# Performance work log

Measured on AMD Instinct MI355X. Metric: run time of the kernel, lower is better.

Reference implementation:

```python
import jax, jax.numpy as jnp
import numpy as np

# Static configuration (mirrors TemporalAugmentation with deterministic choices)
B, T_IN, N, C = 32, 512, 543, 3
SPEED = 1.2                      # fixed draw from speed_range (0.8, 1.2)
NEW_T = int(T_IN / SPEED)        # 426
JITTER_FREQ = max(1, NEW_T // 8) # 53
FRAME_DROP_P = 0.1
JITTER_STD = 0.02
NOISE_STD = 0.01
SPATIAL_STD = 0.005


def linresample(x, out_T):
    """F.interpolate(mode='linear', align_corners=True) along last axis."""
    L = x.shape[-1]
    s = jnp.arange(out_T, dtype=x.dtype) * ((L - 1) / (out_T - 1))
    i0 = jnp.clip(jnp.floor(s).astype(jnp.int32), 0, L - 2)
    frac = s - i0.astype(x.dtype)
    return x[..., i0] * (1 - frac) + x[..., i0 + 1] * frac


def setup_inputs() -> dict:
    key = jax.random.key(0)
    k1, k2, k3, k4, k5 = jax.random.split(key, 5)
    x = jax.random.normal(k1, (B, T_IN, N, C), dtype=jnp.float32)
    mask = jnp.ones((B, T_IN), dtype=bool)
    keep_mask = jax.random.bernoulli(k2, 1.0 - FRAME_DROP_P, (B, NEW_T))
    keep_mask = keep_mask.at[:, 0].set(True).at[:, -1].set(True)
    base_jitter = jax.random.normal(k3, (B, JITTER_FREQ), dtype=jnp.float32)
    noise = jax.random.normal(k4, (B, NEW_T, N, C), dtype=jnp.float32)
    spatial_noise = jax.random.normal(k5, (B, 1, N, C), dtype=jnp.float32)
    return {"x": x, "mask": mask, "keep_mask": keep_mask,
            "base_jitter": base_jitter, "noise": noise,
            "spatial_noise": spatial_noise}


def reference(x, mask, keep_mask, base_jitter, noise, spatial_noise):
    Bb, T, Nn, Cc = x.shape
    # --- speed augment: linear resample time axis T -> NEW_T ---
    xt = jnp.moveaxis(x, 1, -1)                 # (B,N,C,T)
    x = jnp.moveaxis(linresample(xt, NEW_T), -1, 1)  # (B,NEW_T,N,C)
    # nearest resample of validity mask (PyTorch 'nearest': floor(t*in/out))
    nidx = jnp.floor(jnp.arange(NEW_T) * (T / NEW_T)).astype(jnp.int32)
    mask = mask[:, nidx]
    T2 = NEW_T
    # --- frame dropout: replace dropped frames with align_corners linear
    # resample of the kept-frame subsequence (length K) back to T2 ---
    K = keep_mask.sum(axis=1)                   # (B,) kept counts
    ar = jnp.arange(T2)
    # stable order putting kept indices first, in original order
    order = jnp.argsort(jnp.where(keep_mask, ar, T2 + ar), axis=1)  # (B,T2)
    s = ar[None, :].astype(x.dtype) * (K[:, None] - 1).astype(x.dtype) / (T2 - 1)
    r0 = jnp.clip(jnp.floor(s).astype(jnp.int32), 0, (K - 2)[:, None])
    frac = (s - r0.astype(x.dtype))[:, :, None, None]
    bidx = jnp.arange(Bb)[:, None]
    idx0 = jnp.take_along_axis(order, r0, axis=1)
    idx1 = jnp.take_along_axis(order, r0 + 1, axis=1)
    interp = x[bidx, idx0] * (1 - frac) + x[bidx, idx1] * frac
    x = jnp.where(keep_mask[:, :, None, None], x, interp)
    mask = mask & keep_mask
    # --- temporal jitter: scale per-frame velocity by smooth jitter curve ---
    jit = linresample(base_jitter * JITTER_STD, T2)   # (B,T2)
    vel = x[:, 1:] - x[:, :-1]
    x = jnp.concatenate([x[:, :1], x[:, 1:] + vel * jit[:, 1:, None, None]], axis=1)
    # --- coordinate noise + per-landmark spatial noise ---
    x = x + noise * NOISE_STD + spatial_noise * SPATIAL_STD
    return x, mask
```

## Files before the change

kernel.cpp:

```cpp
#include <hip/hip_runtime.h>
#include <stdint.h>

#define B_      32
#define T_IN_   512
#define N_      543
#define C_      3
#define NEW_T_  426
#define JF_     53
#define NC_     (N_*C_)
#define XOUT_   (B_*NEW_T_*NC_)
#define NGROUP_ (XOUT_/4)

#define MODE_INT   0
#define MODE_BYTE  1
#define MODE_FLOAT 2

typedef float f4u __attribute__((vector_size(16), aligned(4)));

__device__ __forceinline__ bool read_flag(const void* p, int mode, int idx) {
    if (mode == MODE_BYTE)  return ((const uint8_t*)p)[idx] != 0;
    if (mode == MODE_FLOAT) return ((const float*)p)[idx]   != 0.0f;
    return ((const int*)p)[idx] != 0;
}

__global__ __launch_bounds__(512) void prep_kernel(
    const void* __restrict__ maskp,
    const void* __restrict__ keepp,
    const float* __restrict__ bjit,
    float* __restrict__ out_mask,
    int4*  __restrict__ wsF,
    float4* __restrict__ wsW,
    float* __restrict__ wsJ)
{
    const int b = blockIdx.x;
    const int tid = threadIdx.x;

    __shared__ int flags[6];
    __shared__ int s_mode_mask, s_mode_keep;
    if (tid < 6) flags[tid] = 0;
    __syncthreads();
    if (tid < 64) {
        uint32_t vm = ((const uint32_t*)maskp)[tid];
        uint32_t vk = ((const uint32_t*)keepp)[tid];
        if (vm == 0x3F800000u)      atomicOr(&flags[2], 1);
        else if (vm > 1u)           atomicOr(&flags[1], 1);
        if (vk == 0x3F800000u)      atomicOr(&flags[5], 1);
        else if (vk > 1u)           atomicOr(&flags[4], 1);
    }
    __syncthreads();
    if (tid == 0) {
        s_mode_mask = flags[2] ? MODE_FLOAT : (flags[1] ? MODE_BYTE : MODE_INT);
        s_mode_keep = flags[5] ? MODE_FLOAT : (flags[4] ? MODE_BYTE : MODE_INT);
    }
    __syncthreads();
    const int mmode = s_mode_mask, kmode = s_mode_keep;

    __shared__ int sk[512];
    __shared__ int ps[512];
    __shared__ int kept[NEW_T_];

    int kv = 0;
    if (tid < NEW_T_) kv = read_flag(keepp, kmode, b*NEW_T_ + tid) ? 1 : 0;
    sk[tid] = (tid < NEW_T_) ? kv : 0;
    ps[tid] = sk[tid];
    __syncthreads();
    for (int off = 1; off < 512; off <<= 1) {
        int v = (tid >= off) ? ps[tid - off] : 0;
        __syncthreads();
        ps[tid] += v;
        __syncthreads();
    }
    const int K = ps[NEW_T_ - 1];
    if (tid < NEW_T_ && kv) kept[ps[tid] - 1] = tid;
    __syncthreads();

    if (tid < NEW_T_) {
        const int t = tid;
        const float RATX = (float)(511.0 / 425.0);
        float st = (float)t * RATX;
        int i0 = (int)floorf(st);
        if (i0 < 0) i0 = 0; if (i0 > T_IN_ - 2) i0 = T_IN_ - 2;
        float w = st - (float)i0;

        int4 F; float4 W;
        if (kv) {
            F = make_int4(i0, i0 + 1, i0, i0 + 1);
            W = make_float4(1.0f - w, w, 0.0f, 0.0f);
        } else {
            float s = ((float)t * (float)(K - 1)) / 425.0f;
            int r0 = (int)floorf(s);
            if (r0 < 0) r0 = 0; if (r0 > K - 2) r0 = K - 2;
            float f = s - (float)r0;
            int j0 = kept[r0], j1 = kept[r0 + 1];
            float s0 = (float)j0 * RATX;
            int a0 = (int)floorf(s0);
            if (a0 < 0) a0 = 0; if (a0 > T_IN_ - 2) a0 = T_IN_ - 2;
            float w0 = s0 - (float)a0;
            float s1 = (float)j1 * RATX;
            int a1 = (int)floorf(s1);
            if (a1 < 0) a1 = 0; if (a1 > T_IN_ - 2) a1 = T_IN_ - 2;
            float w1 = s1 - (float)a1;
            F = make_int4(a0, a0 + 1, a1, a1 + 1);
            W = make_float4((1.0f - f) * (1.0f - w0), (1.0f - f) * w0,
                            f * (1.0f - w1),          f * w1);
        }
        const int bt = b * NEW_T_ + t;
        wsF[bt] = F;
        wsW[bt] = W;

        const float RATJ = (float)(52.0 / 425.0);
        float sj = (float)t * RATJ;
        int ji = (int)floorf(sj);
        if (ji < 0) ji = 0; if (ji > JF_ - 2) ji = JF_ - 2;
        float jf = sj - (float)ji;
        float b0 = bjit[b*JF_ + ji]     * 0.02f;
        float b1 = bjit[b*JF_ + ji + 1] * 0.02f;
        float jv = b0 * (1.0f - jf) + b1 * jf;
        if (t == 0) jv = 0.0f;
        wsJ[bt] = jv;

        float mn = (float)t * (float)(512.0 / 426.0);
        int nidx = (int)floorf(mn);
        if (nidx > T_IN_ - 1) nidx = T_IN_ - 1;
        bool mo = read_flag(maskp, mmode, b*T_IN_ + nidx) && (kv != 0);
        out_mask[bt] = mo ? 1.0f : 0.0f;
    }
}

__global__ __launch_bounds__(256) void main_kernel(
    const float* __restrict__ x,
    const float* __restrict__ noise,
    const float* __restrict__ spat,
    const int4*  __restrict__ wsF,
    const float4* __restrict__ wsW,
    const float* __restrict__ wsJ,
    float* __restrict__ out)
{
    uint32_t g = blockIdx.x * 256u + threadIdx.x;
    if (g >= (uint32_t)NGROUP_) return;
    uint32_t flat = g * 4u;
    uint32_t bt = flat / (uint32_t)NC_;
    uint32_t e  = flat - bt * (uint32_t)NC_;

    if (e <= (uint32_t)(NC_ - 4)) {
        uint32_t b = bt / (uint32_t)NEW_T_;
        const float* xb = x + (size_t)b * (T_IN_ * NC_);
        int4  F  = wsF[bt];  float4 W  = wsW[bt];
        uint32_t pbt = bt ? bt - 1u : 0u;
        int4  FP = wsF[pbt]; float4 WP = wsW[pbt];
        float jv = wsJ[bt];

        f4u t0 = *(const f4u*)(xb + (uint32_t)F.x  * NC_ + e);
        f4u t1 = *(const f4u*)(xb + (uint32_t)F.y  * NC_ + e);
        f4u t2 = *(const f4u*)(xb + (uint32_t)F.z  * NC_ + e);
        f4u t3 = *(const f4u*)(xb + (uint32_t)F.w  * NC_ + e);
        f4u q0 = *(const f4u*)(xb + (uint32_t)FP.x * NC_ + e);
        f4u q1 = *(const f4u*)(xb + (uint32_t)FP.y * NC_ + e);
        f4u q2 = *(const f4u*)(xb + (uint32_t)FP.z * NC_ + e);
        f4u q3 = *(const f4u*)(xb + (uint32_t)FP.w * NC_ + e);
        f4u nz = *(const f4u*)(noise + flat);
        f4u sp = *(const f4u*)(spat + b * NC_ + e);

        f4u a  = W.x  * t0 + W.y  * t1 + W.z  * t2 + W.w  * t3;
        f4u ap = WP.x * q0 + WP.y * q1 + WP.z * q2 + WP.w * q3;
        f4u r  = a + (a - ap) * jv + nz * 0.01f + sp * 0.005f;
        *(f4u*)(out + flat) = r;
    } else {
        #pragma unroll
        for (int i = 0; i < 4; i++) {
            uint32_t fl  = flat + i;
            uint32_t bt2 = fl / (uint32_t)NC_;
            uint32_t e2  = fl - bt2 * (uint32_t)NC_;
            uint32_t b2  = bt2 / (uint32_t)NEW_T_;
            const float* xb = x + (size_t)b2 * (T_IN_ * NC_);
            int4  F  = wsF[bt2];  float4 W  = wsW[bt2];
            uint32_t pbt = bt2 ? bt2 - 1u : 0u;
            int4  FP = wsF[pbt];  float4 WP = wsW[pbt];
            float jv = wsJ[bt2];
            float a  = W.x  * xb[(uint32_t)F.x  * NC_ + e2] + W.y  * xb[(uint32_t)F.y  * NC_ + e2]
                     + W.z  * xb[(uint32_t)F.z  * NC_ + e2] + W.w  * xb[(uint32_t)F.w  * NC_ + e2];
            float ap = WP.x * xb[(uint32_t)FP.x * NC_ + e2] + WP.y * xb[(uint32_t)FP.y * NC_ + e2]
                     + WP.z * xb[(uint32_t)FP.z * NC_ + e2] + WP.w * xb[(uint32_t)FP.w * NC_ + e2];
            out[fl] = a + (a - ap) * jv + noise[fl] * 0.01f + spat[b2 * NC_ + e2] * 0.005f;
        }
    }
}

extern "C" void kernel_launch(void* const* d_in, const int* in_sizes, int n_in,
                              void* d_out, int out_size, void* d_ws, size_t ws_size,
                              hipStream_t stream) {
    const float* x    = (const float*)d_in[0];
    const void*  mask = d_in[1];
    const void*  keep = d_in[2];
    const float* bjit = (const float*)d_in[3];
    const float* noise = (const float*)d_in[4];
    const float* spat  = (const float*)d_in[5];
    float* out = (float*)d_out;

    char* ws = (char*)d_ws;
    int4*   wsF = (int4*)ws;
    float4* wsW = (float4*)(ws + 218112);
    float*  wsJ = (float*)(ws + 436224);

    prep_kernel<<<B_, 512, 0, stream>>>(mask, keep, bjit,
                                        out + XOUT_, wsF, wsW, wsJ);
    const int nblk = (NGROUP_ + 255) / 256;
    main_kernel<<<nblk, 256, 0, stream>>>(x, noise, spat, wsF, wsW, wsJ, out);
}
```

Before: 273.3 us.

## Process four per-frame groups per thread with batched loads and frame-aligned indexing

Reworks the main kernel so each thread handles four 4-element groups strided across the grid. All weight, index and data loads are issued first, then the math and stores run. Indexing is now per frame: 408 groups per frame, with the last group clamped so it overlaps and rewrites three elements, which removes the scalar tail path. Integer divisions become multiply-shift reciprocals, and a waves-per-eu hint is added. The aim is more memory-level parallelism per thread and less index arithmetic, at the cost of higher register pressure and some redundant overlapping writes.

```diff
diff --git a/kernel.cpp b/kernel.cpp
--- a/kernel.cpp
+++ b/kernel.cpp
@@ -9,7 +9,11 @@
 #define JF_     53
 #define NC_     (N_*C_)
 #define XOUT_   (B_*NEW_T_*NC_)
-#define NGROUP_ (XOUT_/4)
+#define NFR_    (B_*NEW_T_)
+#define GPF_    408
+#define TOTG_   (NFR_*GPF_)
+#define G_      4
+#define NBLK_   5432
 
 #define MODE_INT   0
 #define MODE_BYTE  1
@@ -127,7 +131,8 @@
     }
 }
 
-__global__ __launch_bounds__(256) void main_kernel(
+__global__ __launch_bounds__(256) __attribute__((amdgpu_waves_per_eu(2, 8)))
+void main_kernel(
     const float* __restrict__ x,
     const float* __restrict__ noise,
     const float* __restrict__ spat,
@@ -136,53 +141,56 @@
     const float* __restrict__ wsJ,
     float* __restrict__ out)
 {
-    uint32_t g = blockIdx.x * 256u + threadIdx.x;
-    if (g >= (uint32_t)NGROUP_) return;
-    uint32_t flat = g * 4u;
-    uint32_t bt = flat / (uint32_t)NC_;
-    uint32_t e  = flat - bt * (uint32_t)NC_;
-
-    if (e <= (uint32_t)(NC_ - 4)) {
-        uint32_t b = bt / (uint32_t)NEW_T_;
-        const float* xb = x + (size_t)b * (T_IN_ * NC_);
-        int4  F  = wsF[bt];  float4 W  = wsW[bt];
+    const uint32_t S = NBLK_ * 256u;
+    const uint32_t g0 = blockIdx.x * 256u + threadIdx.x;
+
+    int4   F[G_], FP[G_];
+    float4 W[G_], WP[G_];
+    float  JV[G_];
+    uint32_t E0[G_], BT[G_], BB[G_];
+    bool   VA[G_];
+
+    #pragma unroll
+    for (int k = 0; k < G_; k++) {
+        uint32_t gid = g0 + (uint32_t)k * S;
+        bool v = gid < (uint32_t)TOTG_;
+        VA[k] = v;
+        uint32_t gc = v ? gid : 0u;
+        uint32_t bt = (uint32_t)(((uint64_t)gc * 673720361ull) >> 38);
+        uint32_t j  = gc - bt * (uint32_t)GPF_;
+        uint32_t e0 = j * 4u; if (e0 > (uint32_t)(NC_ - 4)) e0 = (uint32_t)(NC_ - 4);
+        uint32_t b  = (uint32_t)(((uint64_t)bt * 161313326ull) >> 36);
         uint32_t pbt = bt ? bt - 1u : 0u;
-        int4  FP = wsF[pbt]; float4 WP = wsW[pbt];
-        float jv = wsJ[bt];
-
-        f4u t0 = *(const f4u*)(xb + (uint32_t)F.x  * NC_ + e);
-        f4u t1 = *(const f4u*)(xb + (uint32_t)F.y  * NC_ + e);
-        f4u t2 = *(const f4u*)(xb + (uint32_t)F.z  * NC_ + e);
-        f4u t3 = *(const f4u*)(xb + (uint32_t)F.w  * NC_ + e);
-        f4u q0 = *(const f4u*)(xb + (uint32_t)FP.x * NC_ + e);
-        f4u q1 = *(const f4u*)(xb + (uint32_t)FP.y * NC_ + e);
-        f4u q2 = *(const f4u*)(xb + (uint32_t)FP.z * NC_ + e);
-        f4u q3 = *(const f4u*)(xb + (uint32_t)FP.w * NC_ + e);
-        f4u nz = *(const f4u*)(noise + flat);
-        f4u sp = *(const f4u*)(spat + b * NC_ + e);
-
-        f4u a  = W.x  * t0 + W.y  * t1 + W.z  * t2 + W.w  * t3;
-        f4u ap = WP.x * q0 + WP.y * q1 + WP.z * q2 + WP.w * q3;
-        f4u r  = a + (a - ap) * jv + nz * 0.01f + sp * 0.005f;
-        *(f4u*)(out + flat) = r;
-    } else {
-        #pragma unroll
-        for (int i = 0; i < 4; i++) {
-            uint32_t fl  = flat + i;
-            uint32_t bt2 = fl / (uint32_t)NC_;
-            uint32_t e2  = fl - bt2 * (uint32_t)NC_;
-            uint32_t b2  = bt2 / (uint32_t)NEW_T_;
-            const float* xb = x + (size_t)b2 * (T_IN_ * NC_);
-            int4  F  = wsF[bt2];  float4 W  = wsW[bt2];
-            uint32_t pbt = bt2 ? bt2 - 1u : 0u;
-            int4  FP = wsF[pbt];  float4 WP = wsW[pbt];
-            float jv = wsJ[bt2];
-            float a  = W.x  * xb[(uint32_t)F.x  * NC_ + e2] + W.y  * xb[(uint32_t)F.y  * NC_ + e2]
-                     + W.z  * xb[(uint32_t)F.z  * NC_ + e2] + W.w  * xb[(uint32_t)F.w  * NC_ + e2];
-            float ap = WP.x * xb[(uint32_t)FP.x * NC_ + e2] + WP.y * xb[(uint32_t)FP.y * NC_ + e2]
-                     + WP.z * xb[(uint32_t)FP.z * NC_ + e2] + WP.w * xb[(uint32_t)FP.w * NC_ + e2];
-            out[fl] = a + (a - ap) * jv + noise[fl] * 0.01f + spat[b2 * NC_ + e2] * 0.005f;
-        }
+        BT[k] = bt; BB[k] = b; E0[k] = e0;
+        F[k]  = wsF[bt];  W[k]  = wsW[bt];
+        FP[k] = wsF[pbt]; WP[k] = wsW[pbt];
+        JV[k] = wsJ[bt];
+    }
+
+    f4u T0[G_], T1[G_], T2[G_], T3[G_], Q0[G_], Q1[G_], Q2[G_], Q3[G_], NZ[G_], SP[G_];
+    #pragma unroll
+    for (int k = 0; k < G_; k++) {
+        const float* xb = x + (size_t)BB[k] * (T_IN_ * NC_);
+        const uint32_t e0 = E0[k];
+        T0[k] = *(const f4u*)(xb + (uint32_t)F[k].x  * NC_ + e0);
+        T1[k] = *(const f4u*)(xb + (uint32_t)F[k].y  * NC_ + e0);
+        T2[k] = *(const f4u*)(xb + (uint32_t)F[k].z  * NC_ + e0);
+        T3[k] = *(const f4u*)(xb + (uint32_t)F[k].w  * NC_ + e0);
+        Q0[k] = *(const f4u*)(xb + (uint32_t)FP[k].x * NC_ + e0);
+        Q1[k] = *(const f4u*)(xb + (uint32_t)FP[k].y * NC_ + e0);
+        Q2[k] = *(const f4u*)(xb + (uint32_t)FP[k].z * NC_ + e0);
+        Q3[k] = *(const f4u*)(xb + (uint32_t)FP[k].w * NC_ + e0);
+        NZ[k] = *(const f4u*)(noise + (size_t)BT[k] * NC_ + e0);
+        SP[k] = *(const f4u*)(spat  + (size_t)BB[k] * NC_ + e0);
+    }
+
+    #pragma unroll
+    for (int k = 0; k < G_; k++) {
+        if (!VA[k]) continue;
+        f4u a  = W[k].x  * T0[k] + W[k].y  * T1[k] + W[k].z  * T2[k] + W[k].w  * T3[k];
+        f4u ap = WP[k].x * Q0[k] + WP[k].y * Q1[k] + WP[k].z * Q2[k] + WP[k].w * Q3[k];
+        f4u r  = a + (a - ap) * JV[k] + NZ[k] * 0.01f + SP[k] * 0.005f;
+        *(f4u*)(out + (size_t)BT[k] * NC_ + E0[k]) = r;
     }
 }
 
@@ -204,6 +212,5 @@
 
     prep_kernel<<<B_, 512, 0, stream>>>(mask, keep, bjit,
                                         out + XOUT_, wsF, wsW, wsJ);
-    const int nblk = (NGROUP_ + 255) / 256;
-    main_kernel<<<nblk, 256, 0, stream>>>(x, noise, spat, wsF, wsW, wsJ, out);
-}
+    main_kernel<<<NBLK_, 256, 0, stream>>>(x, noise, spat, wsF, wsW, wsJ, out);
+}
```

Result: no change. 270.3 us (-1.1%).
